# Optimization experiments

Measured on AMD Instinct MI355X. Metric: run time of the kernel, lower is better.

The kernel has to match this reference:

```python
import jax, jax.numpy as jnp
import numpy as np

C = 2000        # num_classes
D_FEAT = 2048   # memory feature dim (hardcoded in module)
N_V = 20000     # rgb samples
N_I = 20000     # ir samples
T = 1.0
PRED_W, FEAT_W, CONF_W = 0.45, 0.4, 0.15
OT_REG, OT_ITERS = 0.07, 30
HIGH_TH, MID_TH, TOPK = 0.55, 0.25, 3


def setup_inputs() -> dict:
    key = jax.random.key(0)
    k = jax.random.split(key, 6)
    return {
        "vis_logits": jax.random.normal(k[0], (N_V, C), jnp.float32),
        "ir_logits": jax.random.normal(k[1], (N_I, C), jnp.float32),
        "vis_memory": jax.random.normal(k[2], (C, D_FEAT), jnp.float32),
        "ir_memory": jax.random.normal(k[3], (C, D_FEAT), jnp.float32),
        "rgb_ids": jax.random.randint(k[4], (N_V,), 0, C),
        "ir_ids": jax.random.randint(k[5], (N_I,), 0, C),
    }


def _class_stats(scores, labels):
    # per-class mean of softmax scores + entropy (matches _build_class_stats)
    proto_sum = jax.ops.segment_sum(scores, labels, num_segments=C)      # [C, C]
    counts = jax.ops.segment_sum(jnp.ones((scores.shape[0],), scores.dtype), labels, num_segments=C)
    proto = proto_sum / jnp.clip(counts, 1.0)[:, None]
    p = jnp.clip(proto, 1e-12)
    entropy = -(p * jnp.log(p)).sum(axis=1)
    return proto, counts, entropy, counts > 0


def _sinkhorn(cost, a, b, mask_f):
    kernel = jnp.exp(-cost / max(OT_REG, 1e-4)) * mask_f
    eps = 1e-8
    def body(_, uv):
        u, v = uv
        kv = kernel @ v + eps
        u = jnp.where(a > 0, a / kv, 0.0)
        ktu = kernel.T @ u + eps
        v = jnp.where(b > 0, b / ktu, 0.0)
        return (u, v)
    u, v = jax.lax.fori_loop(0, OT_ITERS, body, (jnp.ones_like(a), jnp.ones_like(b)))
    return u[:, None] * kernel * v[None, :] * mask_f


def _topk_mask(m):
    k = min(TOPK, m.shape[1])
    vals, idx = jax.lax.top_k(m, k)
    rows = jnp.arange(m.shape[0])[:, None]
    return jnp.zeros_like(m).at[rows, idx].set(vals)


def reference(vis_logits, ir_logits, vis_memory, ir_memory, rgb_ids, ir_ids):
    # save() in 'scores' mode: temperature softmax
    vis_scores = jax.nn.softmax(T * vis_logits, axis=1)
    ir_scores = jax.nn.softmax(T * ir_logits, axis=1)

    vis_proto, vis_count, vis_ent, vis_active = _class_stats(vis_scores, rgb_ids)
    ir_proto, ir_count, ir_ent, ir_active = _class_stats(ir_scores, ir_ids)

    vmem = vis_memory / jnp.clip(jnp.linalg.norm(vis_memory, axis=1, keepdims=True), 1e-12)
    imem = ir_memory / jnp.clip(jnp.linalg.norm(ir_memory, axis=1, keepdims=True), 1e-12)
    feat_score = jnp.clip((vmem @ imem.T + 1.0) * 0.5, 0.0, 1.0)          # [C, C]
    pred_score = 0.5 * (vis_proto + ir_proto.T)
    conf_score = jnp.clip(
        1.0 - (vis_ent[:, None] + ir_ent[None, :]) / (2.0 * np.log(C + 1e-12)), 0.0, 1.0)

    active = vis_active[:, None] & ir_active[None, :]
    cost = PRED_W * (1.0 - pred_score) + FEAT_W * (1.0 - feat_score) + CONF_W * (1.0 - conf_score)
    masked_max = jnp.max(jnp.where(active, cost, -jnp.inf))
    high = jnp.where(active.any(), masked_max + 1.0, 1.0)
    cost = jnp.where(active, cost, high)

    a = vis_count / jnp.clip(vis_count.sum(), 1.0)
    b = ir_count / jnp.clip(ir_count.sum(), 1.0)
    transport = _sinkhorn(cost, a, b, active.astype(cost.dtype))

    row_t = transport / jnp.clip(transport.sum(axis=1, keepdims=True), 1e-12)
    col_t = transport.T / jnp.clip(transport.T.sum(axis=1, keepdims=True), 1e-12)
    row_conf = row_t.max(axis=1); row_assign = row_t.argmax(axis=1)
    col_conf = col_t.max(axis=1); col_assign = col_t.argmax(axis=1)

    ids = jnp.arange(C)
    mutual_rows = col_assign[row_assign] == ids
    mutual_cols = row_assign[col_assign] == ids
    common_row = vis_active & (row_conf >= HIGH_TH) & mutual_rows
    common_col = ir_active & (col_conf >= HIGH_TH) & mutual_cols
    spec_row = vis_active & (row_conf >= HIGH_TH) & ~common_row
    rem_row = vis_active & (row_conf >= MID_TH) & (row_conf < HIGH_TH)
    rem_col = ir_active & (col_conf >= MID_TH) & (col_conf < HIGH_TH)

    common_rm = jnp.where(common_row[:, None],
                          jax.nn.one_hot(row_assign, C, dtype=row_t.dtype) * row_conf[:, None],
                          0.0)
    specific_rm = row_t * spec_row[:, None].astype(row_t.dtype)
    remain_rm = _topk_mask(row_t * rem_row[:, None].astype(row_t.dtype))
    remain_col_rm = _topk_mask(col_t * rem_col[:, None].astype(col_t.dtype))

    return jnp.stack([row_t, col_t, common_rm, specific_rm, remain_rm, remain_col_rm])
```

## Files before the change

### kernel.cpp

```cpp
#include <hip/hip_runtime.h>

#define CN 2000
#define DF 2048
#define NS 20000
#define NBLK 125
#define NGRP 25
#define GRPSZ 5

typedef __attribute__((ext_vector_type(4))) float          f32x4;
typedef __attribute__((ext_vector_type(4))) int            i32x4;
typedef __attribute__((ext_vector_type(4))) unsigned short u16x4;

__device__ __forceinline__ float wredSum(float v){
#pragma unroll
  for (int o = 32; o >= 1; o >>= 1) v += __shfl_xor(v, o, 64);
  return v;
}
__device__ __forceinline__ float wredMax(float v){
#pragma unroll
  for (int o = 32; o >= 1; o >>= 1) v = fmaxf(v, __shfl_xor(v, o, 64));
  return v;
}
__device__ __forceinline__ unsigned short bfbits(float x){
  union { float f; unsigned u; } c; c.f = x;
  return (unsigned short)((c.u + 0x7fffu + ((c.u >> 16) & 1u)) >> 16);
}
__device__ __forceinline__ void gload16(const void* g, void* lds){
  __builtin_amdgcn_global_load_lds((const __attribute__((address_space(1))) unsigned int*)g,
      (__attribute__((address_space(3))) unsigned int*)lds, 16, 0, 0);
}

__device__ __forceinline__ void gbar(int* bar, int target){
  asm volatile("s_waitcnt vmcnt(0)" ::: "memory");
  __syncthreads();
  if (threadIdx.x == 0){
    int g = blockIdx.x / GRPSZ;
    int prev = __hip_atomic_fetch_add(&bar[64 + g * 32], 1,
                  __ATOMIC_RELAXED, __HIP_MEMORY_SCOPE_AGENT);
    if (prev == target * GRPSZ - 1){
      int rp = __hip_atomic_fetch_add(&bar[0], 1,
                  __ATOMIC_RELAXED, __HIP_MEMORY_SCOPE_AGENT);
      if (rp == target * NGRP - 1){
        __hip_atomic_store(&bar[32], target, __ATOMIC_RELAXED, __HIP_MEMORY_SCOPE_AGENT);
      }
    }
    while (__hip_atomic_load(&bar[32], __ATOMIC_RELAXED, __HIP_MEMORY_SCOPE_AGENT) < target){
      __builtin_amdgcn_s_sleep(1);
    }
  }
  __syncthreads();
}

__global__ void k_zero(int* p, int n, int* bar){
  int i = blockIdx.x * 256 + threadIdx.x;
  if (i < n) p[i] = 0;
  if (i < 1024) bar[i] = 0;
}

__global__ void k_hist(const int* __restrict__ rgb, const int* __restrict__ iri,
                       int* cv, int* ci){
  int i = blockIdx.x * 256 + threadIdx.x;
  if (i < NS) atomicAdd(&cv[rgb[i]], 1);
  else if (i < 2 * NS) atomicAdd(&ci[iri[i - NS]], 1);
}

__global__ __launch_bounds__(1024) void k_scan(const int* __restrict__ cv, const int* __restrict__ ci,
                                               int* ov, int* oi){
  __shared__ int s[2048];
  int t = threadIdx.x;
  for (int pass = 0; pass < 2; ++pass){
    const int* c = pass ? ci : cv;
    int* o = pass ? oi : ov;
    s[t] = (t < CN) ? c[t] : 0;
    s[t + 1024] = (t + 1024 < CN) ? c[t + 1024] : 0;
    __syncthreads();
    for (int off = 1; off < 2048; off <<= 1){
      int a = (t >= off) ? s[t - off] : 0;
      int b = (t + 1024 >= off) ? s[t + 1024 - off] : 0;
      __syncthreads();
      s[t] += a; s[t + 1024] += b;
      __syncthreads();
    }
    if (t < CN) o[t] = s[t] - c[t];
    if (t + 1024 < CN) o[t + 1024] = s[t + 1024] - c[t + 1024];
    __syncthreads();
  }
}

__global__ void k_scatter(const int* __restrict__ rgb, const int* __restrict__ iri,
                          const int* __restrict__ ov, const int* __restrict__ oi,
                          int* curv, int* curi, int* ordv, int* ordi){
  int i = blockIdx.x * 256 + threadIdx.x;
  if (i < NS){
    int l = rgb[i];
    int p = atomicAdd(&curv[l], 1);
    ordv[ov[l] + p] = i;
  } else if (i < 2 * NS){
    int k = i - NS;
    int l = iri[k];
    int p = atomicAdd(&curi[l], 1);
    ordi[oi[l] + p] = k;
  }
}

__global__ __launch_bounds__(256) void k_class(const float* __restrict__ visl, const float* __restrict__ irl,
    const int* __restrict__ cv, const int* __restrict__ ci,
    const int* __restrict__ ov, const int* __restrict__ oi,
    const int* __restrict__ ordv, const int* __restrict__ ordi,
    float* __restrict__ pv, float* __restrict__ pi_,
    float* __restrict__ ev, float* __restrict__ ei,
    const float* __restrict__ vm, const float* __restrict__ im,
    unsigned short* __restrict__ vmb, unsigned short* __restrict__ imb,
    float* __restrict__ rv, float* __restrict__ ri){
  if (blockIdx.x >= 2 * CN){
    int g = (blockIdx.x - 2 * CN) * 256 + threadIdx.x;
    int wid = g >> 6, l = g & 63;
    if (wid >= 2 * CN) return;
    const float* src = (wid < CN) ? vm : im;
    unsigned short* dst = (wid < CN) ? vmb : imb;
    int r = (wid < CN) ? wid : wid - CN;
    const f32x4* row = (const f32x4*)(src + (size_t)r * DF);
    float s = 0.f;
#pragma unroll
    for (int k = 0; k < 8; ++k){
      int idx = l + k * 64;
      f32x4 vv = row[idx];
      s += vv[0]*vv[0] + vv[1]*vv[1] + vv[2]*vv[2] + vv[3]*vv[3];
      u16x4 o;
      o[0] = bfbits(vv[0]); o[1] = bfbits(vv[1]); o[2] = bfbits(vv[2]); o[3] = bfbits(vv[3]);
      *(u16x4*)(dst + (size_t)r * DF + idx * 4) = o;
    }
    s = wredSum(s);
    if (l == 0) ((wid < CN) ? rv : ri)[r] = 1.f / fmaxf(sqrtf(s), 1e-12f);
    return;
  }
  __shared__ __attribute__((aligned(16))) float acc4[4][2048];
  __shared__ int mem[128];
  __shared__ float red[4];
  int t = threadIdx.x, w = t >> 6, l = t & 63;
  bool ir = (blockIdx.x >= CN);
  int c = ir ? blockIdx.x - CN : blockIdx.x;
  const float* logits = ir ? irl : visl;
  int n = (ir ? ci : cv)[c];
  int base = (ir ? oi : ov)[c];
  const int* ord = ir ? ordi : ordv;
  float* proto = ir ? pi_ : pv;
  float* ent = ir ? ei : ev;
  bool useL = (n <= 128);
  for (int m = t; m < n && m < 128; m += 256) mem[m] = ord[base + m];
  for (int j = t; j < 2048; j += 256){
    acc4[0][j] = 0.f; acc4[1][j] = 0.f; acc4[2][j] = 0.f; acc4[3][j] = 0.f;
  }
  __syncthreads();
  if (t == 0 && useL){
    for (int a = 1; a < n; ++a){
      int key = mem[a]; int b = a - 1;
      while (b >= 0 && mem[b] > key){ mem[b + 1] = mem[b]; --b; }
      mem[b + 1] = key;
    }
  }
  __syncthreads();
  for (int m = w; m < n; m += 4){
    int sidx = useL ? mem[m] : ord[base + m];
    const f32x4* row = (const f32x4*)(logits + (size_t)sidx * CN);
    f32x4 x[8]; float mx = -3.0e38f;
#pragma unroll
    for (int k = 0; k < 8; ++k){
      int idx = l + k * 64;
      f32x4 vv = {-3.0e38f, -3.0e38f, -3.0e38f, -3.0e38f};
      if (idx < 500) vv = row[idx];
      x[k] = vv;
      mx = fmaxf(mx, fmaxf(fmaxf(vv[0], vv[1]), fmaxf(vv[2], vv[3])));
    }
    mx = wredMax(mx);
    float sm = 0.f;
#pragma unroll
    for (int k = 0; k < 8; ++k){
      int idx = l + k * 64;
      if (idx < 500){
        f32x4 e;
        e[0] = expf(x[k][0] - mx); e[1] = expf(x[k][1] - mx);
        e[2] = expf(x[k][2] - mx); e[3] = expf(x[k][3] - mx);
        x[k] = e;
        sm += e[0] + e[1] + e[2] + e[3];
      }
    }
    sm = wredSum(sm);
    float inv = 1.f / sm;
#pragma unroll
    for (int k = 0; k < 8; ++k){
      int idx = l + k * 64;
      if (idx < 500){
        f32x4* a = (f32x4*)&acc4[w][idx * 4];
        f32x4 cur = *a;
        cur[0] += x[k][0] * inv; cur[1] += x[k][1] * inv;
        cur[2] += x[k][2] * inv; cur[3] += x[k][3] * inv;
        *a = cur;
      }
    }
  }
  __syncthreads();
  float invc = 1.f / fmaxf((float)n, 1.f);
  float el = 0.f;
  for (int j = t; j < CN; j += 256){
    float p = (acc4[0][j] + acc4[1][j] + acc4[2][j] + acc4[3][j]) * invc;
    proto[(size_t)c * CN + j] = p;
    p = fmaxf(p, 1e-12f);
    el -= p * logf(p);
  }
  el = wredSum(el);
  if (l == 0) red[w] = el;
  __syncthreads();
  if (t == 0) ent[c] = red[0] + red[1] + red[2] + red[3];
}

__global__ __launch_bounds__(256) void k_prep(const float* __restrict__ pv, const float* __restrict__ pi_,
    const float* __restrict__ ev, const float* __restrict__ ei,
    const int* __restrict__ cv, const int* __restrict__ ci, float* __restrict__ E){
  __shared__ float s[64][65];
  int t = threadIdx.x;
  int i0 = blockIdx.y * 64, j0 = blockIdx.x * 64;
#pragma unroll
  for (int rr = 0; rr < 4; ++rr){
    int jl = (t >> 4) + rr * 16;
    int ch = t & 15;
    int gj = j0 + jl;
    int gib = i0 + ch * 4;
    f32x4 vv = {0.f, 0.f, 0.f, 0.f};
    if (gj < CN){
      if (gib + 3 < CN) vv = *(const f32x4*)(pi_ + (size_t)gj * CN + gib);
      else {
        for (int q = 0; q < 4; ++q) if (gib + q < CN) vv[q] = pi_[(size_t)gj * CN + gib + q];
      }
    }
    s[ch*4+0][jl] = vv[0]; s[ch*4+1][jl] = vv[1]; s[ch*4+2][jl] = vv[2]; s[ch*4+3][jl] = vv[3];
  }
  __syncthreads();
#pragma unroll
  for (int rr = 0; rr < 4; ++rr){
    int il = (t >> 4) + rr * 16;
    int ch = t & 15;
    int gi = i0 + il;
    int gjb = j0 + ch * 4;
    if (gi >= CN) continue;
    f32x4 pvv = {0.f, 0.f, 0.f, 0.f};
    bool full = (gjb + 3 < CN);
    if (full) pvv = *(const f32x4*)(pv + (size_t)gi * CN + gjb);
    else { for (int q = 0; q < 4; ++q) if (gjb + q < CN) pvv[q] = pv[(size_t)gi * CN + gjb + q]; }
    float evi = ev[gi];
    bool avi = cv[gi] > 0;
    f32x4 o;
#pragma unroll
    for (int q = 0; q < 4; ++q){
      int gj = gjb + q;
      if (gj >= CN){ o[q] = 0.f; continue; }
      float pred = 0.5f * (pvv[q] + s[il][ch*4+q]);
      float conf = fminf(fmaxf(1.f - (evi + ei[gj]) / 15.201804919084164f, 0.f), 1.f);
      float base = 0.45f * (1.f - pred) + 0.15f * (1.f - conf);
      bool act = avi && (ci[gj] > 0);
      o[q] = act ? expf(-base / 0.07f) : 0.f;
    }
    if (full) *(f32x4*)(E + (size_t)gi * CN + gjb) = o;
    else { for (int q = 0; q < 4; ++q) if (gjb + q < CN) E[(size_t)gi * CN + gjb + q] = o[q]; }
  }
}

__global__ __launch_bounds__(256) void k_gemm2(const unsigned short* __restrict__ Ag,
    const unsigned short* __restrict__ Bg, const float* __restrict__ rv,
    const float* __restrict__ ri, const float* __restrict__ E, float* __restrict__ Km){
  __shared__ __attribute__((aligned(16))) unsigned short As[128 * 64];
  __shared__ __attribute__((aligned(16))) unsigned short Bs[128 * 64];
  int t = threadIdx.x, w = t >> 6, l = t & 63;
  int i0 = blockIdx.y * 128, j0 = blockIdx.x * 128;
  int wm = w >> 1, wn = w & 1;
  int srow8 = l >> 3, sch = l & 7;
  int lr = l & 15, hk = l >> 4;
  f32x4 z = {0.f, 0.f, 0.f, 0.f};
  f32x4 acc[4][4];
#pragma unroll
  for (int a = 0; a < 4; ++a)
#pragma unroll
    for (int b = 0; b < 4; ++b) acc[a][b] = z;

  for (int kt = 0; kt < DF / 64; ++kt){
    int k0 = kt * 64;
#pragma unroll
    for (int c2 = 0; c2 < 4; ++c2){
      int rbase = c2 * 32 + w * 8;
      int row = rbase + srow8;
      int lch = sch ^ (srow8 & 7);
      int gi = i0 + row; if (gi > CN - 1) gi = CN - 1;
      int gj = j0 + row; if (gj > CN - 1) gj = CN - 1;
      gload16(Ag + (size_t)gi * DF + k0 + lch * 8, &As[rbase * 64]);
      gload16(Bg + (size_t)gj * DF + k0 + lch * 8, &Bs[rbase * 64]);
    }
    __syncthreads();
#pragma unroll
    for (int s2 = 0; s2 < 2; ++s2){
      i32x4 af[4], bf[4];
#pragma unroll
      for (int f2 = 0; f2 < 4; ++f2){
        int ar = wm * 64 + f2 * 16 + lr;
        int ac = (s2 * 4 + hk) ^ (ar & 7);
        af[f2] = *(const i32x4*)&As[ar * 64 + ac * 8];
        int br = wn * 64 + f2 * 16 + lr;
        int bc = (s2 * 4 + hk) ^ (br & 7);
        bf[f2] = *(const i32x4*)&Bs[br * 64 + bc * 8];
      }
#pragma unroll
      for (int a = 0; a < 4; ++a)
#pragma unroll
        for (int b = 0; b < 4; ++b)
          asm volatile("v_mfma_f32_16x16x32_bf16 %0, %1, %2, %0"
                       : "+v"(acc[a][b]) : "v"(af[a]), "v"(bf[b]));
    }
    __syncthreads();
  }
#pragma unroll
  for (int a = 0; a < 4; ++a){
    int ib = i0 + wm * 64 + a * 16 + hk * 4;
#pragma unroll
    for (int b = 0; b < 4; ++b){
      int j = j0 + wn * 64 + b * 16 + lr;
      if (j < CN){
        float rij = ri[j];
#pragma unroll
        for (int q = 0; q < 4; ++q){
          int i = ib + q;
          if (i < CN){
            float dot = acc[a][b][q] * rv[i] * rij;
            float feat = fminf(fmaxf((dot + 1.f) * 0.5f, 0.f), 1.f);
            float kv = E[(size_t)i * CN + j] * expf(-0.4f * (1.f - feat) / 0.07f);
            Km[(size_t)i * CN + j] = kv;
          }
        }
      }
    }
  }
}

__global__ __launch_bounds__(256) void k_tr(const float* __restrict__ Km, float* __restrict__ KT){
  __shared__ float s[64][65];
  int t = threadIdx.x;
  int i0 = blockIdx.y * 64, j0 = blockIdx.x * 64;
#pragma unroll
  for (int rr = 0; rr < 4; ++rr){
    int il = (t >> 4) + rr * 16;
    int ch = t & 15;
    int gi = i0 + il, gjb = j0 + ch * 4;
    f32x4 vv = {0.f, 0.f, 0.f, 0.f};
    if (gi < CN){
      if (gjb + 3 < CN) vv = *(const f32x4*)(Km + (size_t)gi * CN + gjb);
      else { for (int q = 0; q < 4; ++q) if (gjb + q < CN) vv[q] = Km[(size_t)gi * CN + gjb + q]; }
    }
    s[ch*4+0][il] = vv[0]; s[ch*4+1][il] = vv[1]; s[ch*4+2][il] = vv[2]; s[ch*4+3][il] = vv[3];
  }
  __syncthreads();
#pragma unroll
  for (int rr = 0; rr < 4; ++rr){
    int jl = (t >> 4) + rr * 16;
    int ch = t & 15;
    int gj = j0 + jl, gib = i0 + ch * 4;
    if (gj >= CN) continue;
    f32x4 o;
    o[0] = s[jl][ch*4+0]; o[1] = s[jl][ch*4+1]; o[2] = s[jl][ch*4+2]; o[3] = s[jl][ch*4+3];
    if (gib + 3 < CN) *(f32x4*)(KT + (size_t)gj * CN + gib) = o;
    else { for (int q = 0; q < 4; ++q) if (gib + q < CN) KT[(size_t)gj * CN + gib + q] = o[q]; }
  }
}

#define STAGE(G, L) do { \
  float tmp_[4]; \
  _Pragma("unroll") \
  for (int k_ = 0; k_ < 4; ++k_){ \
    int idx_ = t + k_ * 512; \
    tmp_[k_] = (idx_ < CN) ? __hip_atomic_load(&(G)[idx_], __ATOMIC_RELAXED, __HIP_MEMORY_SCOPE_AGENT) : 0.f; \
  } \
  _Pragma("unroll") \
  for (int k_ = 0; k_ < 4; ++k_){ int idx_ = t + k_ * 512; if (idx_ < CN) (L)[idx_] = tmp_[k_]; } \
} while(0)

__global__ __launch_bounds__(512, 1) void k_sink(
    const float* __restrict__ Km, const float* __restrict__ KTm,
    const int* __restrict__ cv, const int* __restrict__ ci,
    float* __restrict__ u_g, float* __restrict__ v_g,
    float* __restrict__ o0, float* __restrict__ o1,
    float* __restrict__ rconf, float* __restrict__ cconf,
    int* __restrict__ rass, int* __restrict__ cass,
    int* bar){
  __shared__ __attribute__((aligned(16))) float u_lds[2048];
  __shared__ __attribute__((aligned(16))) float v_lds[2048];
  int b = blockIdx.x, t = threadIdx.x, w = t >> 6, l = t & 63;
  int r0 = b * 16 + w * 2, r1 = r0 + 1;
  f32x4 z4 = {0.f, 0.f, 0.f, 0.f};
  f32x4 kA0[8], kA1[8], kT0[8], kT1[8];
  {
    const f32x4* g0 = (const f32x4*)(Km + (size_t)r0 * CN);
    const f32x4* g1 = (const f32x4*)(Km + (size_t)r1 * CN);
    const f32x4* h0 = (const f32x4*)(KTm + (size_t)r0 * CN);
    const f32x4* h1 = (const f32x4*)(KTm + (size_t)r1 * CN);
#pragma unroll
    for (int k = 0; k < 8; ++k){
      int idx = l + k * 64;
      bool ok = idx < 500;
      kA0[k] = ok ? g0[idx] : z4;
      kA1[k] = ok ? g1[idx] : z4;
      kT0[k] = ok ? h0[idx] : z4;
      kT1[k] = ok ? h1[idx] : z4;
    }
  }
  float a0 = (float)cv[r0] / 20000.0f, a1 = (float)cv[r1] / 20000.0f;
  float b0 = (float)ci[r0] / 20000.0f, b1 = (float)ci[r1] / 20000.0f;

  {
    float s0 = 0.f, s1 = 0.f;
#pragma unroll
    for (int k = 0; k < 8; ++k){
      s0 += kA0[k][0] + kA0[k][1] + kA0[k][2] + kA0[k][3];
      s1 += kA1[k][0] + kA1[k][1] + kA1[k][2] + kA1[k][3];
    }
    s0 = wredSum(s0); s1 = wredSum(s1);
    if (l == 0){
      __hip_atomic_store(&u_g[r0], (a0 > 0.f) ? a0 / (s0 + 1e-8f) : 0.f,
                         __ATOMIC_RELAXED, __HIP_MEMORY_SCOPE_AGENT);
      __hip_atomic_store(&u_g[r1], (a1 > 0.f) ? a1 / (s1 + 1e-8f) : 0.f,
                         __ATOMIC_RELAXED, __HIP_MEMORY_SCOPE_AGENT);
    }
  }
  int tgt = 1;
  gbar(bar, tgt); ++tgt;
  STAGE(u_g, u_lds);
  __syncthreads();
  const f32x4* ul4 = (const f32x4*)u_lds;
  const f32x4* vl4 = (const f32x4*)v_lds;

  for (int it = 0; it < 30; ++it){
    {
      float s0 = 0.f, s1 = 0.f;
#pragma unroll
      for (int k = 0; k < 8; ++k){
        int idx = l + k * 64;
        if (idx < 500){
          f32x4 x = ul4[idx];
          s0 += kT0[k][0]*x[0] + kT0[k][1]*x[1] + kT0[k][2]*x[2] + kT0[k][3]*x[3];
          s1 += kT1[k][0]*x[0] + kT1[k][1]*x[1] + kT1[k][2]*x[2] + kT1[k][3]*x[3];
        }
      }
      s0 = wredSum(s0); s1 = wredSum(s1);
      if (l == 0){
        __hip_atomic_store(&v_g[r0], (b0 > 0.f) ? b0 / (s0 + 1e-8f) : 0.f,
                           __ATOMIC_RELAXED, __HIP_MEMORY_SCOPE_AGENT);
        __hip_atomic_store(&v_g[r1], (b1 > 0.f) ? b1 / (s1 + 1e-8f) : 0.f,
                           __ATOMIC_RELAXED, __HIP_MEMORY_SCOPE_AGENT);
      }
    }
    gbar(bar, tgt); ++tgt;
    STAGE(v_g, v_lds);
    __syncthreads();
    if (it < 29){
      {
        float s0 = 0.f, s1 = 0.f;
#pragma unroll
        for (int k = 0; k < 8; ++k){
          int idx = l + k * 64;
          if (idx < 500){
            f32x4 x = vl4[idx];
            s0 += kA0[k][0]*x[0] + kA0[k][1]*x[1] + kA0[k][2]*x[2] + kA0[k][3]*x[3];
            s1 += kA1[k][0]*x[0] + kA1[k][1]*x[1] + kA1[k][2]*x[2] + kA1[k][3]*x[3];
          }
        }
        s0 = wredSum(s0); s1 = wredSum(s1);
        if (l == 0){
          __hip_atomic_store(&u_g[r0], (a0 > 0.f) ? a0 / (s0 + 1e-8f) : 0.f,
                             __ATOMIC_RELAXED, __HIP_MEMORY_SCOPE_AGENT);
          __hip_atomic_store(&u_g[r1], (a1 > 0.f) ? a1 / (s1 + 1e-8f) : 0.f,
                             __ATOMIC_RELAXED, __HIP_MEMORY_SCOPE_AGENT);
        }
      }
      gbar(bar, tgt); ++tgt;
      STAGE(u_g, u_lds);
      __syncthreads();
    }
  }
  {
    float s0 = 0.f, s1 = 0.f;
#pragma unroll
    for (int k = 0; k < 8; ++k){
      int idx = l + k * 64;
      if (idx < 500){
        f32x4 x = vl4[idx];
        s0 += kA0[k][0]*x[0] + kA0[k][1]*x[1] + kA0[k][2]*x[2] + kA0[k][3]*x[3];
        s1 += kA1[k][0]*x[0] + kA1[k][1]*x[1] + kA1[k][2]*x[2] + kA1[k][3]*x[3];
      }
    }
    s0 = wredSum(s0); s1 = wredSum(s1);
    float uu0 = u_lds[r0], uu1 = u_lds[r1];
    float f0 = uu0 * (1.f / fmaxf(uu0 * s0, 1e-12f));
    float f1 = uu1 * (1.f / fmaxf(uu1 * s1, 1e-12f));
    float bm0 = -1e30f, bm1 = -1e30f; int bi0 = 1 << 30, bi1 = 1 << 30;
    f32x4* d0 = (f32x4*)(o0 + (size_t)r0 * CN);
    f32x4* d1 = (f32x4*)(o0 + (size_t)r1 * CN);
#pragma unroll
    for (int k = 0; k < 8; ++k){
      int idx = l + k * 64;
      if (idx < 500){
        f32x4 x = vl4[idx];
        f32x4 w0, w1;
#pragma unroll
        for (int q = 0; q < 4; ++q){
          w0[q] = f0 * kA0[k][q] * x[q];
          w1[q] = f1 * kA1[k][q] * x[q];
        }
        d0[idx] = w0; d1[idx] = w1;
#pragma unroll
        for (int q = 0; q < 4; ++q){
          int j = idx * 4 + q;
          if (w0[q] > bm0){ bm0 = w0[q]; bi0 = j; }
          if (w1[q] > bm1){ bm1 = w1[q]; bi1 = j; }
        }
      }
    }
#pragma unroll
    for (int o = 32; o >= 1; o >>= 1){
      float om = __shfl_xor(bm0, o, 64); int oi2 = __shfl_xor(bi0, o, 64);
      if (om > bm0 || (om == bm0 && oi2 < bi0)){ bm0 = om; bi0 = oi2; }
      float om1 = __shfl_xor(bm1, o, 64); int oi3 = __shfl_xor(bi1, o, 64);
      if (om1 > bm1 || (om1 == bm1 && oi3 < bi1)){ bm1 = om1; bi1 = oi3; }
    }
    if (l == 0){ rconf[r0] = bm0; rass[r0] = bi0; rconf[r1] = bm1; rass[r1] = bi1; }
  }
  {
    float s0 = 0.f, s1 = 0.f;
#pragma unroll
    for (int k = 0; k < 8; ++k){
      int idx = l + k * 64;
      if (idx < 500){
        f32x4 x = ul4[idx];
        s0 += kT0[k][0]*x[0] + kT0[k][1]*x[1] + kT0[k][2]*x[2] + kT0[k][3]*x[3];
        s1 += kT1[k][0]*x[0] + kT1[k][1]*x[1] + kT1[k][2]*x[2] + kT1[k][3]*x[3];
      }
    }
    s0 = wredSum(s0); s1 = wredSum(s1);
    float vv0 = v_lds[r0], vv1 = v_lds[r1];
    float f0 = vv0 * (1.f / fmaxf(vv0 * s0, 1e-12f));
    float f1 = vv1 * (1.f / fmaxf(vv1 * s1, 1e-12f));
    float bm0 = -1e30f, bm1 = -1e30f; int bi0 = 1 << 30, bi1 = 1 << 30;
    f32x4* d0 = (f32x4*)(o1 + (size_t)r0 * CN);
    f32x4* d1 = (f32x4*)(o1 + (size_t)r1 * CN);
#pragma unroll
    for (int k = 0; k < 8; ++k){
      int idx = l + k * 64;
      if (idx < 500){
        f32x4 x = ul4[idx];
        f32x4 w0, w1;
#pragma unroll
        for (int q = 0; q < 4; ++q){
          w0[q] = f0 * kT0[k][q] * x[q];
          w1[q] = f1 * kT1[k][q] * x[q];
        }
        d0[idx] = w0; d1[idx] = w1;
#pragma unroll
        for (int q = 0; q < 4; ++q){
          int j = idx * 4 + q;
          if (w0[q] > bm0){ bm0 = w0[q]; bi0 = j; }
          if (w1[q] > bm1){ bm1 = w1[q]; bi1 = j; }
        }
      }
    }
#pragma unroll
    for (int o = 32; o >= 1; o >>= 1){
      float om = __shfl_xor(bm0, o, 64); int oi2 = __shfl_xor(bi0, o, 64);
      if (om > bm0 || (om == bm0 && oi2 < bi0)){ bm0 = om; bi0 = oi2; }
      float om1 = __shfl_xor(bm1, o, 64); int oi3 = __shfl_xor(bi1, o, 64);
      if (om1 > bm1 || (om1 == bm1 && oi3 < bi1)){ bm1 = om1; bi1 = oi3; }
    }
    if (l == 0){ cconf[r0] = bm0; cass[r0] = bi0; cconf[r1] = bm1; cass[r1] = bi1; }
  }
}

__global__ __launch_bounds__(256) void k_post(const float* __restrict__ rt, const float* __restrict__ ct,
    const int* __restrict__ cv, const int* __restrict__ ci,
    const float* __restrict__ rc, const float* __restrict__ cc,
    const int* __restrict__ ra, const int* __restrict__ ca,
    float* o2, float* o3, float* o4, float* o5){
  __shared__ float sv[256 * 3];
  __shared__ int si[256 * 3];
  int i = blockIdx.x, t = threadIdx.x;
  bool av = cv[i] > 0, ai = ci[i] > 0;
  float rcv = rc[i], ccv = cc[i];
  int aidx = ra[i];
  bool high = av && (rcv >= 0.55f);
  bool cm = high && (ca[aidx] == i);
  bool sp = high && !cm;
  bool remr = av && (rcv >= 0.25f) && (rcv < 0.55f);
  bool remc = ai && (ccv >= 0.25f) && (ccv < 0.55f);
  f32x4 z = {0.f, 0.f, 0.f, 0.f};
  f32x4* p2 = (f32x4*)(o2 + (size_t)i * CN);
  f32x4* p3 = (f32x4*)(o3 + (size_t)i * CN);
  f32x4* p4 = (f32x4*)(o4 + (size_t)i * CN);
  f32x4* p5 = (f32x4*)(o5 + (size_t)i * CN);
  const f32x4* rp = (const f32x4*)(rt + (size_t)i * CN);
  for (int c = t; c < 500; c += 256){
    p2[c] = z;
    p3[c] = sp ? rp[c] : z;
    p4[c] = z;
    p5[c] = z;
  }
  __syncthreads();
  if (t == 0 && cm) o2[(size_t)i * CN + aidx] = rcv;
  for (int pass = 0; pass < 2; ++pass){
    bool run = pass ? remc : remr;
    if (!run) continue;
    const float* M = pass ? ct : rt;
    float* o = pass ? o5 : o4;
    float v0 = -1.f, v1 = -1.f, v2 = -1.f;
    int i0 = 1 << 30, i1 = 1 << 30, i2 = 1 << 30;
    for (int k = 0; k < 8; ++k){
      int j = t + k * 256;
      if (j >= CN) break;
      float val = M[(size_t)i * CN + j];
      if (val > v0 || (val == v0 && j < i0)){ v2=v1; i2=i1; v1=v0; i1=i0; v0=val; i0=j; }
      else if (val > v1 || (val == v1 && j < i1)){ v2=v1; i2=i1; v1=val; i1=j; }
      else if (val > v2 || (val == v2 && j < i2)){ v2=val; i2=j; }
    }
    sv[t*3+0]=v0; sv[t*3+1]=v1; sv[t*3+2]=v2;
    si[t*3+0]=i0; si[t*3+1]=i1; si[t*3+2]=i2;
    __syncthreads();
    if (t == 0){
      float w0=-1.f, w1=-1.f, w2=-1.f; int j0=1<<30, j1=1<<30, j2=1<<30;
      for (int q = 0; q < 256 * 3; ++q){
        float val = sv[q]; int j = si[q];
        if (j >= CN) continue;
        if (val > w0 || (val == w0 && j < j0)){ w2=w1; j2=j1; w1=w0; j1=j0; w0=val; j0=j; }
        else if (val > w1 || (val == w1 && j < j1)){ w2=w1; j2=j1; w1=val; j1=j; }
        else if (val > w2 || (val == w2 && j < j2)){ w2=val; j2=j; }
      }
      o[(size_t)i * CN + j0] = w0;
      o[(size_t)i * CN + j1] = w1;
      o[(size_t)i * CN + j2] = w2;
    }
    __syncthreads();
  }
}

extern "C" void kernel_launch(void* const* d_in, const int* in_sizes, int n_in,
                              void* d_out, int out_size, void* d_ws, size_t ws_size,
                              hipStream_t stream){
  (void)in_sizes; (void)n_in; (void)out_size; (void)ws_size;
  const float* visl = (const float*)d_in[0];
  const float* irl  = (const float*)d_in[1];
  const float* vm   = (const float*)d_in[2];
  const float* im   = (const float*)d_in[3];
  const int* rgb    = (const int*)d_in[4];
  const int* iri    = (const int*)d_in[5];
  float* out = (float*)d_out;
  float* o0 = out;
  float* o1 = out + 4000000;
  float* o2 = out + 8000000;
  float* o3 = out + 12000000;
  float* o4 = out + 16000000;
  float* o5 = out + 20000000;
  char* sm = (char*)d_ws;
  float* ev   = (float*)(sm + 0);
  float* ei   = (float*)(sm + 8000);
  float* rv   = (float*)(sm + 16000);
  float* ri   = (float*)(sm + 24000);
  float* uvec = (float*)(sm + 32000);
  float* vvec = (float*)(sm + 40000);
  int* bar    = (int*)(sm + 48000);
  float* rconf= (float*)(sm + 64000);
  float* cconf= (float*)(sm + 72000);
  int* rass = (int*)(sm + 80000);
  int* cass = (int*)(sm + 88000);
  int* cv   = (int*)(sm + 96000);
  int* ci   = (int*)(sm + 104000);
  int* ov   = (int*)(sm + 112000);
  int* oi   = (int*)(sm + 120000);
  int* curv = (int*)(sm + 128000);
  int* curi = (int*)(sm + 136000);
  int* ordv = (int*)(sm + 176000);
  int* ordi = (int*)(sm + 256000);
  unsigned short* vmb = (unsigned short*)o5;
  unsigned short* imb = (unsigned short*)o1;

  k_zero<<<47, 256, 0, stream>>>(cv, 12000, bar);
  k_hist<<<157, 256, 0, stream>>>(rgb, iri, cv, ci);
  k_scan<<<1, 1024, 0, stream>>>(cv, ci, ov, oi);
  k_scatter<<<157, 256, 0, stream>>>(rgb, iri, ov, oi, curv, curi, ordv, ordi);
  k_class<<<2 * CN + 1000, 256, 0, stream>>>(visl, irl, cv, ci, ov, oi, ordv, ordi,
                                             o2, o3, ev, ei, vm, im, vmb, imb, rv, ri);
  k_prep<<<dim3(32, 32), 256, 0, stream>>>(o2, o3, ev, ei, cv, ci, o4);
  k_gemm2<<<dim3(16, 16), 256, 0, stream>>>(vmb, imb, rv, ri, o4, o0);
  k_tr<<<dim3(32, 32), 256, 0, stream>>>(o0, o1);
  k_sink<<<NBLK, 512, 0, stream>>>(o0, o1, cv, ci, uvec, vvec, o0, o1,
                                   rconf, cconf, rass, cass, bar);
  k_post<<<CN, 256, 0, stream>>>(o0, o1, cv, ci, rconf, cconf, rass, cass, o2, o3, o4, o5);
}
```

Measured before the change: 423.2 us.

## Replace grid barriers in Sinkhorn with tagged per-element flag publication

```diff
diff --git a/kernel.cpp b/kernel.cpp
--- a/kernel.cpp
+++ b/kernel.cpp
@@ -4,12 +4,11 @@
 #define DF 2048
 #define NS 20000
 #define NBLK 125
-#define NGRP 25
-#define GRPSZ 5
 
 typedef __attribute__((ext_vector_type(4))) float          f32x4;
 typedef __attribute__((ext_vector_type(4))) int            i32x4;
 typedef __attribute__((ext_vector_type(4))) unsigned short u16x4;
+typedef unsigned long long u64;
 
 __device__ __forceinline__ float wredSum(float v){
 #pragma unroll
@@ -30,31 +29,10 @@
       (__attribute__((address_space(3))) unsigned int*)lds, 16, 0, 0);
 }
 
-__device__ __forceinline__ void gbar(int* bar, int target){
-  asm volatile("s_waitcnt vmcnt(0)" ::: "memory");
-  __syncthreads();
-  if (threadIdx.x == 0){
-    int g = blockIdx.x / GRPSZ;
-    int prev = __hip_atomic_fetch_add(&bar[64 + g * 32], 1,
-                  __ATOMIC_RELAXED, __HIP_MEMORY_SCOPE_AGENT);
-    if (prev == target * GRPSZ - 1){
-      int rp = __hip_atomic_fetch_add(&bar[0], 1,
-                  __ATOMIC_RELAXED, __HIP_MEMORY_SCOPE_AGENT);
-      if (rp == target * NGRP - 1){
-        __hip_atomic_store(&bar[32], target, __ATOMIC_RELAXED, __HIP_MEMORY_SCOPE_AGENT);
-      }
-    }
-    while (__hip_atomic_load(&bar[32], __ATOMIC_RELAXED, __HIP_MEMORY_SCOPE_AGENT) < target){
-      __builtin_amdgcn_s_sleep(1);
-    }
-  }
-  __syncthreads();
-}
-
-__global__ void k_zero(int* p, int n, int* bar){
+__global__ void k_zero(int* p, int n, int* pk, int npk){
   int i = blockIdx.x * 256 + threadIdx.x;
   if (i < n) p[i] = 0;
-  if (i < 1024) bar[i] = 0;
+  if (i < npk) pk[i] = 0;
 }
 
 __global__ void k_hist(const int* __restrict__ rgb, const int* __restrict__ iri,
@@ -369,25 +347,42 @@
   }
 }
 
-#define STAGE(G, L) do { \
-  float tmp_[4]; \
-  _Pragma("unroll") \
-  for (int k_ = 0; k_ < 4; ++k_){ \
-    int idx_ = t + k_ * 512; \
-    tmp_[k_] = (idx_ < CN) ? __hip_atomic_load(&(G)[idx_], __ATOMIC_RELAXED, __HIP_MEMORY_SCOPE_AGENT) : 0.f; \
+#define PUBLISH(PK, ROW, VAL, TAG) \
+  __hip_atomic_store(&(PK)[ROW], \
+      ((u64)(unsigned)(TAG) << 32) | (u64)__float_as_uint(VAL), \
+      __ATOMIC_RELAXED, __HIP_MEMORY_SCOPE_AGENT)
+
+#define GATHER(PK, L, TAG) do { \
+  float vals_[4]; int got_[4] = {0,0,0,0}; \
+  int need_ = 4; \
+  while (need_ > 0){ \
+    need_ = 0; \
+    _Pragma("unroll") \
+    for (int k_ = 0; k_ < 4; ++k_){ \
+      int idx_ = t + k_ * 512; \
+      if (!got_[k_]){ \
+        if (idx_ >= CN){ vals_[k_] = 0.f; got_[k_] = 1; } \
+        else { \
+          u64 w_ = __hip_atomic_load(&(PK)[idx_], __ATOMIC_RELAXED, __HIP_MEMORY_SCOPE_AGENT); \
+          if ((unsigned)(w_ >> 32) == (unsigned)(TAG)){ \
+            vals_[k_] = __uint_as_float((unsigned)w_); got_[k_] = 1; \
+          } else ++need_; \
+        } \
+      } \
+    } \
+    if (need_) __builtin_amdgcn_s_sleep(2); \
   } \
   _Pragma("unroll") \
-  for (int k_ = 0; k_ < 4; ++k_){ int idx_ = t + k_ * 512; if (idx_ < CN) (L)[idx_] = tmp_[k_]; } \
+  for (int k_ = 0; k_ < 4; ++k_){ int idx_ = t + k_ * 512; if (idx_ < CN) (L)[idx_] = vals_[k_]; } \
 } while(0)
 
 __global__ __launch_bounds__(512, 1) void k_sink(
     const float* __restrict__ Km, const float* __restrict__ KTm,
     const int* __restrict__ cv, const int* __restrict__ ci,
-    float* __restrict__ u_g, float* __restrict__ v_g,
+    u64* __restrict__ upk, u64* __restrict__ vpk,
     float* __restrict__ o0, float* __restrict__ o1,
     float* __restrict__ rconf, float* __restrict__ cconf,
-    int* __restrict__ rass, int* __restrict__ cass,
-    int* bar){
+    int* __restrict__ rass, int* __restrict__ cass){
   __shared__ __attribute__((aligned(16))) float u_lds[2048];
   __shared__ __attribute__((aligned(16))) float v_lds[2048];
   int b = blockIdx.x, t = threadIdx.x, w = t >> 6, l = t & 63;
@@ -421,20 +416,16 @@
     }
     s0 = wredSum(s0); s1 = wredSum(s1);
     if (l == 0){
-      __hip_atomic_store(&u_g[r0], (a0 > 0.f) ? a0 / (s0 + 1e-8f) : 0.f,
-                         __ATOMIC_RELAXED, __HIP_MEMORY_SCOPE_AGENT);
-      __hip_atomic_store(&u_g[r1], (a1 > 0.f) ? a1 / (s1 + 1e-8f) : 0.f,
-                         __ATOMIC_RELAXED, __HIP_MEMORY_SCOPE_AGENT);
-    }
-  }
-  int tgt = 1;
-  gbar(bar, tgt); ++tgt;
-  STAGE(u_g, u_lds);
-  __syncthreads();
+      PUBLISH(upk, r0, (a0 > 0.f) ? a0 / (s0 + 1e-8f) : 0.f, 1);
+      PUBLISH(upk, r1, (a1 > 0.f) ? a1 / (s1 + 1e-8f) : 0.f, 1);
+    }
+  }
   const f32x4* ul4 = (const f32x4*)u_lds;
   const f32x4* vl4 = (const f32x4*)v_lds;
 
-  for (int it = 0; it < 30; ++it){
+  for (int it = 1; it <= 30; ++it){
+    GATHER(upk, u_lds, it);
+    __syncthreads();
     {
       float s0 = 0.f, s1 = 0.f;
 #pragma unroll
@@ -448,40 +439,32 @@
       }
       s0 = wredSum(s0); s1 = wredSum(s1);
       if (l == 0){
-        __hip_atomic_store(&v_g[r0], (b0 > 0.f) ? b0 / (s0 + 1e-8f) : 0.f,
-                           __ATOMIC_RELAXED, __HIP_MEMORY_SCOPE_AGENT);
-        __hip_atomic_store(&v_g[r1], (b1 > 0.f) ? b1 / (s1 + 1e-8f) : 0.f,
-                           __ATOMIC_RELAXED, __HIP_MEMORY_SCOPE_AGENT);
-      }
-    }
-    gbar(bar, tgt); ++tgt;
-    STAGE(v_g, v_lds);
-    __syncthreads();
-    if (it < 29){
-      {
-        float s0 = 0.f, s1 = 0.f;
-#pragma unroll
-        for (int k = 0; k < 8; ++k){
-          int idx = l + k * 64;
-          if (idx < 500){
-            f32x4 x = vl4[idx];
-            s0 += kA0[k][0]*x[0] + kA0[k][1]*x[1] + kA0[k][2]*x[2] + kA0[k][3]*x[3];
-            s1 += kA1[k][0]*x[0] + kA1[k][1]*x[1] + kA1[k][2]*x[2] + kA1[k][3]*x[3];
-          }
+        PUBLISH(vpk, r0, (b0 > 0.f) ? b0 / (s0 + 1e-8f) : 0.f, it);
+        PUBLISH(vpk, r1, (b1 > 0.f) ? b1 / (s1 + 1e-8f) : 0.f, it);
+      }
+    }
+    if (it < 30){
+      GATHER(vpk, v_lds, it);
+      __syncthreads();
+      float s0 = 0.f, s1 = 0.f;
+#pragma unroll
+      for (int k = 0; k < 8; ++k){
+        int idx = l + k * 64;
+        if (idx < 500){
+          f32x4 x = vl4[idx];
+          s0 += kA0[k][0]*x[0] + kA0[k][1]*x[1] + kA0[k][2]*x[2] + kA0[k][3]*x[3];
+          s1 += kA1[k][0]*x[0] + kA1[k][1]*x[1] + kA1[k][2]*x[2] + kA1[k][3]*x[3];
         }
-        s0 = wredSum(s0); s1 = wredSum(s1);
-        if (l == 0){
-          __hip_atomic_store(&u_g[r0], (a0 > 0.f) ? a0 / (s0 + 1e-8f) : 0.f,
-                             __ATOMIC_RELAXED, __HIP_MEMORY_SCOPE_AGENT);
-          __hip_atomic_store(&u_g[r1], (a1 > 0.f) ? a1 / (s1 + 1e-8f) : 0.f,
-                             __ATOMIC_RELAXED, __HIP_MEMORY_SCOPE_AGENT);
-        }
-      }
-      gbar(bar, tgt); ++tgt;
-      STAGE(u_g, u_lds);
-      __syncthreads();
-    }
-  }
+      }
+      s0 = wredSum(s0); s1 = wredSum(s1);
+      if (l == 0){
+        PUBLISH(upk, r0, (a0 > 0.f) ? a0 / (s0 + 1e-8f) : 0.f, it + 1);
+        PUBLISH(upk, r1, (a1 > 0.f) ? a1 / (s1 + 1e-8f) : 0.f, it + 1);
+      }
+    }
+  }
+  GATHER(vpk, v_lds, 30);
+  __syncthreads();
   {
     float s0 = 0.f, s1 = 0.f;
 #pragma unroll
@@ -665,25 +648,24 @@
   float* ei   = (float*)(sm + 8000);
   float* rv   = (float*)(sm + 16000);
   float* ri   = (float*)(sm + 24000);
-  float* uvec = (float*)(sm + 32000);
-  float* vvec = (float*)(sm + 40000);
-  int* bar    = (int*)(sm + 48000);
-  float* rconf= (float*)(sm + 64000);
-  float* cconf= (float*)(sm + 72000);
-  int* rass = (int*)(sm + 80000);
-  int* cass = (int*)(sm + 88000);
-  int* cv   = (int*)(sm + 96000);
-  int* ci   = (int*)(sm + 104000);
-  int* ov   = (int*)(sm + 112000);
-  int* oi   = (int*)(sm + 120000);
-  int* curv = (int*)(sm + 128000);
-  int* curi = (int*)(sm + 136000);
+  u64* upk    = (u64*)(sm + 32000);
+  u64* vpk    = (u64*)(sm + 48384);
+  float* rconf= (float*)(sm + 65536);
+  float* cconf= (float*)(sm + 73536);
+  int* rass = (int*)(sm + 81536);
+  int* cass = (int*)(sm + 89536);
+  int* cv   = (int*)(sm + 98304);
+  int* ci   = (int*)(sm + 106304);
+  int* ov   = (int*)(sm + 114304);
+  int* oi   = (int*)(sm + 122304);
+  int* curv = (int*)(sm + 130304);
+  int* curi = (int*)(sm + 138304);
   int* ordv = (int*)(sm + 176000);
   int* ordi = (int*)(sm + 256000);
   unsigned short* vmb = (unsigned short*)o5;
   unsigned short* imb = (unsigned short*)o1;
 
-  k_zero<<<47, 256, 0, stream>>>(cv, 12000, bar);
+  k_zero<<<47, 256, 0, stream>>>(cv, 12000, (int*)upk, 8192);
   k_hist<<<157, 256, 0, stream>>>(rgb, iri, cv, ci);
   k_scan<<<1, 1024, 0, stream>>>(cv, ci, ov, oi);
   k_scatter<<<157, 256, 0, stream>>>(rgb, iri, ov, oi, curv, curi, ordv, ordi);
@@ -692,7 +674,7 @@
   k_prep<<<dim3(32, 32), 256, 0, stream>>>(o2, o3, ev, ei, cv, ci, o4);
   k_gemm2<<<dim3(16, 16), 256, 0, stream>>>(vmb, imb, rv, ri, o4, o0);
   k_tr<<<dim3(32, 32), 256, 0, stream>>>(o0, o1);
-  k_sink<<<NBLK, 512, 0, stream>>>(o0, o1, cv, ci, uvec, vvec, o0, o1,
-                                   rconf, cconf, rass, cass, bar);
+  k_sink<<<NBLK, 512, 0, stream>>>(o0, o1, cv, ci, upk, vpk, o0, o1,
+                                   rconf, cconf, rass, cass);
   k_post<<<CN, 256, 0, stream>>>(o0, o1, cv, ci, rconf, cconf, rass, cass, o2, o3, o4, o5);
 }
```

After: 435.0 us. 2.8% more time.

## Fuse post-processing into Sinkhorn kernel and swizzle GEMM block order

Applied to the files above, without the earlier changes.

```diff
diff --git a/kernel.cpp b/kernel.cpp
--- a/kernel.cpp
+++ b/kernel.cpp
@@ -271,7 +271,9 @@
   __shared__ __attribute__((aligned(16))) unsigned short As[128 * 64];
   __shared__ __attribute__((aligned(16))) unsigned short Bs[128 * 64];
   int t = threadIdx.x, w = t >> 6, l = t & 63;
-  int i0 = blockIdx.y * 128, j0 = blockIdx.x * 128;
+  int bid = blockIdx.y * 16 + blockIdx.x;
+  int swz = (bid & 7) * 32 + (bid >> 3);
+  int i0 = (swz >> 4) * 128, j0 = (swz & 15) * 128;
   int wm = w >> 1, wn = w & 1;
   int srow8 = l >> 3, sch = l & 7;
   int lr = l & 15, hk = l >> 4;
@@ -380,14 +382,20 @@
   for (int k_ = 0; k_ < 4; ++k_){ int idx_ = t + k_ * 512; if (idx_ < CN) (L)[idx_] = tmp_[k_]; } \
 } while(0)
 
+#define INS3(V0,V1,V2,I0,I1,I2,cvx,cjx) do { \
+  float cv_ = (cvx); int cj_ = (cjx); \
+  if (cv_ > V0 || (cv_ == V0 && cj_ < I0)){ V2=V1;I2=I1; V1=V0;I1=I0; V0=cv_;I0=cj_; } \
+  else if (cv_ > V1 || (cv_ == V1 && cj_ < I1)){ V2=V1;I2=I1; V1=cv_;I1=cj_; } \
+  else if (cv_ > V2 || (cv_ == V2 && cj_ < I2)){ V2=cv_;I2=cj_; } \
+} while(0)
+
 __global__ __launch_bounds__(512, 1) void k_sink(
     const float* __restrict__ Km, const float* __restrict__ KTm,
     const int* __restrict__ cv, const int* __restrict__ ci,
     float* __restrict__ u_g, float* __restrict__ v_g,
     float* __restrict__ o0, float* __restrict__ o1,
-    float* __restrict__ rconf, float* __restrict__ cconf,
-    int* __restrict__ rass, int* __restrict__ cass,
-    int* bar){
+    int* __restrict__ cass, int* bar,
+    float* o2, float* o3, float* o4, float* o5){
   __shared__ __attribute__((aligned(16))) float u_lds[2048];
   __shared__ __attribute__((aligned(16))) float v_lds[2048];
   int b = blockIdx.x, t = threadIdx.x, w = t >> 6, l = t & 63;
@@ -482,6 +490,9 @@
       __syncthreads();
     }
   }
+  float rf0, rf1;
+  float rA0 = -1.f, rA1 = -1.f, rA2 = -1.f; int iA0 = 1<<30, iA1 = 1<<30, iA2 = 1<<30;
+  float rB0 = -1.f, rB1 = -1.f, rB2 = -1.f; int iB0 = 1<<30, iB1 = 1<<30, iB2 = 1<<30;
   {
     float s0 = 0.f, s1 = 0.f;
 #pragma unroll
@@ -495,9 +506,8 @@
     }
     s0 = wredSum(s0); s1 = wredSum(s1);
     float uu0 = u_lds[r0], uu1 = u_lds[r1];
-    float f0 = uu0 * (1.f / fmaxf(uu0 * s0, 1e-12f));
-    float f1 = uu1 * (1.f / fmaxf(uu1 * s1, 1e-12f));
-    float bm0 = -1e30f, bm1 = -1e30f; int bi0 = 1 << 30, bi1 = 1 << 30;
+    rf0 = uu0 * (1.f / fmaxf(uu0 * s0, 1e-12f));
+    rf1 = uu1 * (1.f / fmaxf(uu1 * s1, 1e-12f));
     f32x4* d0 = (f32x4*)(o0 + (size_t)r0 * CN);
     f32x4* d1 = (f32x4*)(o0 + (size_t)r1 * CN);
 #pragma unroll
@@ -508,27 +518,35 @@
         f32x4 w0, w1;
 #pragma unroll
         for (int q = 0; q < 4; ++q){
-          w0[q] = f0 * kA0[k][q] * x[q];
-          w1[q] = f1 * kA1[k][q] * x[q];
+          w0[q] = rf0 * kA0[k][q] * x[q];
+          w1[q] = rf1 * kA1[k][q] * x[q];
         }
         d0[idx] = w0; d1[idx] = w1;
 #pragma unroll
         for (int q = 0; q < 4; ++q){
           int j = idx * 4 + q;
-          if (w0[q] > bm0){ bm0 = w0[q]; bi0 = j; }
-          if (w1[q] > bm1){ bm1 = w1[q]; bi1 = j; }
+          INS3(rA0, rA1, rA2, iA0, iA1, iA2, w0[q], j);
+          INS3(rB0, rB1, rB2, iB0, iB1, iB2, w1[q], j);
         }
       }
     }
 #pragma unroll
     for (int o = 32; o >= 1; o >>= 1){
-      float om = __shfl_xor(bm0, o, 64); int oi2 = __shfl_xor(bi0, o, 64);
-      if (om > bm0 || (om == bm0 && oi2 < bi0)){ bm0 = om; bi0 = oi2; }
-      float om1 = __shfl_xor(bm1, o, 64); int oi3 = __shfl_xor(bi1, o, 64);
-      if (om1 > bm1 || (om1 == bm1 && oi3 < bi1)){ bm1 = om1; bi1 = oi3; }
-    }
-    if (l == 0){ rconf[r0] = bm0; rass[r0] = bi0; rconf[r1] = bm1; rass[r1] = bi1; }
-  }
+      float q0 = __shfl_xor(rA0, o, 64), q1 = __shfl_xor(rA1, o, 64), q2 = __shfl_xor(rA2, o, 64);
+      int p0 = __shfl_xor(iA0, o, 64), p1 = __shfl_xor(iA1, o, 64), p2 = __shfl_xor(iA2, o, 64);
+      float y0 = __shfl_xor(rB0, o, 64), y1 = __shfl_xor(rB1, o, 64), y2 = __shfl_xor(rB2, o, 64);
+      int z0 = __shfl_xor(iB0, o, 64), z1 = __shfl_xor(iB1, o, 64), z2 = __shfl_xor(iB2, o, 64);
+      INS3(rA0, rA1, rA2, iA0, iA1, iA2, q0, p0);
+      INS3(rA0, rA1, rA2, iA0, iA1, iA2, q1, p1);
+      INS3(rA0, rA1, rA2, iA0, iA1, iA2, q2, p2);
+      INS3(rB0, rB1, rB2, iB0, iB1, iB2, y0, z0);
+      INS3(rB0, rB1, rB2, iB0, iB1, iB2, y1, z1);
+      INS3(rB0, rB1, rB2, iB0, iB1, iB2, y2, z2);
+    }
+  }
+  float cf0, cf1;
+  float cA0 = -1.f, cA1 = -1.f, cA2 = -1.f; int jA0 = 1<<30, jA1 = 1<<30, jA2 = 1<<30;
+  float cB0 = -1.f, cB1 = -1.f, cB2 = -1.f; int jB0 = 1<<30, jB1 = 1<<30, jB2 = 1<<30;
   {
     float s0 = 0.f, s1 = 0.f;
 #pragma unroll
@@ -542,9 +560,8 @@
     }
     s0 = wredSum(s0); s1 = wredSum(s1);
     float vv0 = v_lds[r0], vv1 = v_lds[r1];
-    float f0 = vv0 * (1.f / fmaxf(vv0 * s0, 1e-12f));
-    float f1 = vv1 * (1.f / fmaxf(vv1 * s1, 1e-12f));
-    float bm0 = -1e30f, bm1 = -1e30f; int bi0 = 1 << 30, bi1 = 1 << 30;
+    cf0 = vv0 * (1.f / fmaxf(vv0 * s0, 1e-12f));
+    cf1 = vv1 * (1.f / fmaxf(vv1 * s1, 1e-12f));
     f32x4* d0 = (f32x4*)(o1 + (size_t)r0 * CN);
     f32x4* d1 = (f32x4*)(o1 + (size_t)r1 * CN);
 #pragma unroll
@@ -555,91 +572,85 @@
         f32x4 w0, w1;
 #pragma unroll
         for (int q = 0; q < 4; ++q){
-          w0[q] = f0 * kT0[k][q] * x[q];
-          w1[q] = f1 * kT1[k][q] * x[q];
+          w0[q] = cf0 * kT0[k][q] * x[q];
+          w1[q] = cf1 * kT1[k][q] * x[q];
         }
         d0[idx] = w0; d1[idx] = w1;
 #pragma unroll
         for (int q = 0; q < 4; ++q){
           int j = idx * 4 + q;
-          if (w0[q] > bm0){ bm0 = w0[q]; bi0 = j; }
-          if (w1[q] > bm1){ bm1 = w1[q]; bi1 = j; }
+          INS3(cA0, cA1, cA2, jA0, jA1, jA2, w0[q], j);
+          INS3(cB0, cB1, cB2, jB0, jB1, jB2, w1[q], j);
         }
       }
     }
 #pragma unroll
     for (int o = 32; o >= 1; o >>= 1){
-      float om = __shfl_xor(bm0, o, 64); int oi2 = __shfl_xor(bi0, o, 64);
-      if (om > bm0 || (om == bm0 && oi2 < bi0)){ bm0 = om; bi0 = oi2; }
-      float om1 = __shfl_xor(bm1, o, 64); int oi3 = __shfl_xor(bi1, o, 64);
-      if (om1 > bm1 || (om1 == bm1 && oi3 < bi1)){ bm1 = om1; bi1 = oi3; }
-    }
-    if (l == 0){ cconf[r0] = bm0; cass[r0] = bi0; cconf[r1] = bm1; cass[r1] = bi1; }
-  }
-}
-
-__global__ __launch_bounds__(256) void k_post(const float* __restrict__ rt, const float* __restrict__ ct,
-    const int* __restrict__ cv, const int* __restrict__ ci,
-    const float* __restrict__ rc, const float* __restrict__ cc,
-    const int* __restrict__ ra, const int* __restrict__ ca,
-    float* o2, float* o3, float* o4, float* o5){
-  __shared__ float sv[256 * 3];
-  __shared__ int si[256 * 3];
-  int i = blockIdx.x, t = threadIdx.x;
-  bool av = cv[i] > 0, ai = ci[i] > 0;
-  float rcv = rc[i], ccv = cc[i];
-  int aidx = ra[i];
-  bool high = av && (rcv >= 0.55f);
-  bool cm = high && (ca[aidx] == i);
-  bool sp = high && !cm;
-  bool remr = av && (rcv >= 0.25f) && (rcv < 0.55f);
-  bool remc = ai && (ccv >= 0.25f) && (ccv < 0.55f);
-  f32x4 z = {0.f, 0.f, 0.f, 0.f};
-  f32x4* p2 = (f32x4*)(o2 + (size_t)i * CN);
-  f32x4* p3 = (f32x4*)(o3 + (size_t)i * CN);
-  f32x4* p4 = (f32x4*)(o4 + (size_t)i * CN);
-  f32x4* p5 = (f32x4*)(o5 + (size_t)i * CN);
-  const f32x4* rp = (const f32x4*)(rt + (size_t)i * CN);
-  for (int c = t; c < 500; c += 256){
-    p2[c] = z;
-    p3[c] = sp ? rp[c] : z;
-    p4[c] = z;
-    p5[c] = z;
-  }
-  __syncthreads();
-  if (t == 0 && cm) o2[(size_t)i * CN + aidx] = rcv;
-  for (int pass = 0; pass < 2; ++pass){
-    bool run = pass ? remc : remr;
-    if (!run) continue;
-    const float* M = pass ? ct : rt;
-    float* o = pass ? o5 : o4;
-    float v0 = -1.f, v1 = -1.f, v2 = -1.f;
-    int i0 = 1 << 30, i1 = 1 << 30, i2 = 1 << 30;
-    for (int k = 0; k < 8; ++k){
-      int j = t + k * 256;
-      if (j >= CN) break;
-      float val = M[(size_t)i * CN + j];
-      if (val > v0 || (val == v0 && j < i0)){ v2=v1; i2=i1; v1=v0; i1=i0; v0=val; i0=j; }
-      else if (val > v1 || (val == v1 && j < i1)){ v2=v1; i2=i1; v1=val; i1=j; }
-      else if (val > v2 || (val == v2 && j < i2)){ v2=val; i2=j; }
-    }
-    sv[t*3+0]=v0; sv[t*3+1]=v1; sv[t*3+2]=v2;
-    si[t*3+0]=i0; si[t*3+1]=i1; si[t*3+2]=i2;
-    __syncthreads();
-    if (t == 0){
-      float w0=-1.f, w1=-1.f, w2=-1.f; int j0=1<<30, j1=1<<30, j2=1<<30;
-      for (int q = 0; q < 256 * 3; ++q){
-        float val = sv[q]; int j = si[q];
-        if (j >= CN) continue;
-        if (val > w0 || (val == w0 && j < j0)){ w2=w1; j2=j1; w1=w0; j1=j0; w0=val; j0=j; }
-        else if (val > w1 || (val == w1 && j < j1)){ w2=w1; j2=j1; w1=val; j1=j; }
-        else if (val > w2 || (val == w2 && j < j2)){ w2=val; j2=j; }
-      }
-      o[(size_t)i * CN + j0] = w0;
-      o[(size_t)i * CN + j1] = w1;
-      o[(size_t)i * CN + j2] = w2;
-    }
-    __syncthreads();
+      float q0 = __shfl_xor(cA0, o, 64), q1 = __shfl_xor(cA1, o, 64), q2 = __shfl_xor(cA2, o, 64);
+      int p0 = __shfl_xor(jA0, o, 64), p1 = __shfl_xor(jA1, o, 64), p2 = __shfl_xor(jA2, o, 64);
+      float y0 = __shfl_xor(cB0, o, 64), y1 = __shfl_xor(cB1, o, 64), y2 = __shfl_xor(cB2, o, 64);
+      int z0 = __shfl_xor(jB0, o, 64), z1 = __shfl_xor(jB1, o, 64), z2 = __shfl_xor(jB2, o, 64);
+      INS3(cA0, cA1, cA2, jA0, jA1, jA2, q0, p0);
+      INS3(cA0, cA1, cA2, jA0, jA1, jA2, q1, p1);
+      INS3(cA0, cA1, cA2, jA0, jA1, jA2, q2, p2);
+      INS3(cB0, cB1, cB2, jB0, jB1, jB2, y0, z0);
+      INS3(cB0, cB1, cB2, jB0, jB1, jB2, y1, z1);
+      INS3(cB0, cB1, cB2, jB0, jB1, jB2, y2, z2);
+    }
+  }
+  if (l == 0){
+    __hip_atomic_store(&cass[r0], jA0, __ATOMIC_RELAXED, __HIP_MEMORY_SCOPE_AGENT);
+    __hip_atomic_store(&cass[r1], jB0, __ATOMIC_RELAXED, __HIP_MEMORY_SCOPE_AGENT);
+  }
+  gbar(bar, tgt); ++tgt;
+  bool av0 = a0 > 0.f, av1 = a1 > 0.f;
+  bool aiA = b0 > 0.f, aiB = b1 > 0.f;
+  bool hi0 = av0 && (rA0 >= 0.55f), hi1 = av1 && (rB0 >= 0.55f);
+  int caA = __hip_atomic_load(&cass[iA0 < CN ? iA0 : 0], __ATOMIC_RELAXED, __HIP_MEMORY_SCOPE_AGENT);
+  int caB = __hip_atomic_load(&cass[iB0 < CN ? iB0 : 0], __ATOMIC_RELAXED, __HIP_MEMORY_SCOPE_AGENT);
+  bool cm0 = hi0 && (caA == r0), cm1 = hi1 && (caB == r1);
+  bool sp0 = hi0 && !cm0, sp1 = hi1 && !cm1;
+  bool rr0 = av0 && (rA0 >= 0.25f) && (rA0 < 0.55f);
+  bool rr1 = av1 && (rB0 >= 0.25f) && (rB0 < 0.55f);
+  bool rc0 = aiA && (cA0 >= 0.25f) && (cA0 < 0.55f);
+  bool rc1 = aiB && (cB0 >= 0.25f) && (cB0 < 0.55f);
+  {
+    f32x4* p2a = (f32x4*)(o2 + (size_t)r0 * CN);
+    f32x4* p2b = (f32x4*)(o2 + (size_t)r1 * CN);
+    f32x4* p3a = (f32x4*)(o3 + (size_t)r0 * CN);
+    f32x4* p3b = (f32x4*)(o3 + (size_t)r1 * CN);
+    f32x4* p4a = (f32x4*)(o4 + (size_t)r0 * CN);
+    f32x4* p4b = (f32x4*)(o4 + (size_t)r1 * CN);
+    f32x4* p5a = (f32x4*)(o5 + (size_t)r0 * CN);
+    f32x4* p5b = (f32x4*)(o5 + (size_t)r1 * CN);
+#pragma unroll
+    for (int k = 0; k < 8; ++k){
+      int idx = l + k * 64;
+      if (idx < 500){
+        f32x4 xv = vl4[idx], xu = ul4[idx];
+        f32x4 e2a, e2b, e3a, e3b, e4a, e4b, e5a, e5b;
+#pragma unroll
+        for (int q = 0; q < 4; ++q){
+          int j = idx * 4 + q;
+          float w0 = rf0 * kA0[k][q] * xv[q];
+          float w1 = rf1 * kA1[k][q] * xv[q];
+          float c0 = cf0 * kT0[k][q] * xu[q];
+          float c1 = cf1 * kT1[k][q] * xu[q];
+          e2a[q] = (cm0 && j == iA0) ? rA0 : 0.f;
+          e2b[q] = (cm1 && j == iB0) ? rB0 : 0.f;
+          e3a[q] = sp0 ? w0 : 0.f;
+          e3b[q] = sp1 ? w1 : 0.f;
+          e4a[q] = (rr0 && (j == iA0 || j == iA1 || j == iA2)) ? w0 : 0.f;
+          e4b[q] = (rr1 && (j == iB0 || j == iB1 || j == iB2)) ? w1 : 0.f;
+          e5a[q] = (rc0 && (j == jA0 || j == jA1 || j == jA2)) ? c0 : 0.f;
+          e5b[q] = (rc1 && (j == jB0 || j == jB1 || j == jB2)) ? c1 : 0.f;
+        }
+        p2a[idx] = e2a; p2b[idx] = e2b;
+        p3a[idx] = e3a; p3b[idx] = e3b;
+        p4a[idx] = e4a; p4b[idx] = e4b;
+        p5a[idx] = e5a; p5b[idx] = e5b;
+      }
+    }
   }
 }
 
@@ -668,9 +679,6 @@
   float* uvec = (float*)(sm + 32000);
   float* vvec = (float*)(sm + 40000);
   int* bar    = (int*)(sm + 48000);
-  float* rconf= (float*)(sm + 64000);
-  float* cconf= (float*)(sm + 72000);
-  int* rass = (int*)(sm + 80000);
   int* cass = (int*)(sm + 88000);
   int* cv   = (int*)(sm + 96000);
   int* ci   = (int*)(sm + 104000);
@@ -693,6 +701,5 @@
   k_gemm2<<<dim3(16, 16), 256, 0, stream>>>(vmb, imb, rv, ri, o4, o0);
   k_tr<<<dim3(32, 32), 256, 0, stream>>>(o0, o1);
   k_sink<<<NBLK, 512, 0, stream>>>(o0, o1, cv, ci, uvec, vvec, o0, o1,
-                                   rconf, cconf, rass, cass, bar);
-  k_post<<<CN, 256, 0, stream>>>(o0, o1, cv, ci, rconf, cconf, rass, cass, o2, o3, o4, o5);
-}
+                                   cass, bar, o2, o3, o4, o5);
+}
```

New measurement: 584.7 us. 1.38x slower.
